# Kernel optimization log

Hardware: AMD Instinct MI355X
Metric: run time of the kernel (lower is better)

The kernel has to match this reference:

```python
import jax, jax.numpy as jnp
import numpy as np
from jax import lax

B, T = 64, 200
NUM_C, DIM_S, SIZE_M = 2000, 128, 50


def setup_inputs() -> dict:
    key = jax.random.key(0)
    ks = jax.random.split(key, 12)
    d = {}
    d['skill'] = jax.random.randint(ks[0], (B, T), 0, NUM_C)
    d['answer'] = jax.random.randint(ks[1], (B, T), 0, 2)
    s = 1.0 / np.sqrt(DIM_S)
    d['k_emb'] = jax.random.normal(ks[2], (NUM_C + 1, DIM_S), jnp.float32)
    d['v_emb'] = jax.random.normal(ks[3], (2 * NUM_C + 1, DIM_S), jnp.float32)
    # kaiming_normal on [size_m, dim_s]: std = sqrt(2/dim_s)
    d['Mk'] = jax.random.normal(ks[4], (SIZE_M, DIM_S), jnp.float32) * np.sqrt(2.0 / DIM_S)
    d['Mv0'] = jax.random.normal(ks[5], (SIZE_M, DIM_S), jnp.float32) * np.sqrt(2.0 / DIM_S)
    d['f_W'] = jax.random.normal(ks[6], (DIM_S, 2 * DIM_S), jnp.float32) * (1.0 / np.sqrt(2 * DIM_S))
    d['f_b'] = jnp.zeros((DIM_S,), jnp.float32)
    d['p_W'] = jax.random.normal(ks[7], (NUM_C, DIM_S), jnp.float32) * s
    d['p_b'] = jnp.zeros((NUM_C,), jnp.float32)
    d['e_W'] = jax.random.normal(ks[8], (DIM_S, DIM_S), jnp.float32) * s
    d['e_b'] = jnp.zeros((DIM_S,), jnp.float32)
    d['a_W'] = jax.random.normal(ks[9], (DIM_S, DIM_S), jnp.float32) * s
    d['a_b'] = jnp.zeros((DIM_S,), jnp.float32)
    return d


def reference(skill, answer, k_emb, v_emb, Mk, Mv0, f_W, f_b, p_W, p_b, e_W, e_b, a_W, a_b):
    num_c = p_W.shape[0]
    bsz = skill.shape[0]
    answer_x = jnp.where(answer == 2, 1, answer)
    x = skill + num_c * answer_x                       # [B,T]
    k = k_emb[skill]                                   # [B,T,D]
    v = v_emb[x]                                       # [B,T,D]
    w = jax.nn.softmax(jnp.einsum('btd,md->btm', k, Mk), axis=-1)   # [B,T,M]
    e = jax.nn.sigmoid(jnp.einsum('btd,ed->bte', v, e_W) + e_b)      # [B,T,D]
    a = jnp.tanh(jnp.einsum('btd,ed->bte', v, a_W) + a_b)            # [B,T,D]

    Mv_init = jnp.broadcast_to(Mv0, (bsz,) + Mv0.shape)              # [B,M,D]

    def step(Mvt, inp):
        et, at, wt = inp                               # [B,D],[B,D],[B,M]
        # read uses pre-update memory (Mv[:, :-1] in the torch code)
        read = jnp.einsum('bm,bmd->bd', wt, Mvt)
        Mvt_new = Mvt * (1.0 - wt[:, :, None] * et[:, None, :]) + wt[:, :, None] * at[:, None, :]
        return Mvt_new, read

    _, reads = lax.scan(step, Mv_init,
                        (e.transpose(1, 0, 2), a.transpose(1, 0, 2), w.transpose(1, 0, 2)))
    reads = reads.transpose(1, 0, 2)                   # [B,T,D]

    f = jnp.tanh(jnp.concatenate([reads, k], axis=-1) @ f_W.T + f_b)  # [B,T,D]
    p = jax.nn.sigmoid(f @ p_W.T + p_b)                # [B,T,num_c] (dropout is identity at eval)
    p = p[:, :-1, :]
    next_skill = skill[:, 1:]                          # [B,T-1]
    idx = jnp.minimum(next_skill, num_c - 1)
    pred = jnp.take_along_axis(p, idx[..., None], axis=-1)[..., 0]
    pred = jnp.where(next_skill < num_c, pred, 0.0)    # index num_c -> zero row in torch one_hot
    return pred
```

## Files before the change

### kernel.cpp

```cpp
#include <hip/hip_runtime.h>
#include <math.h>

#define Bsz 64
#define Tn 200
#define NUMC 2000
#define DS 128
#define SM 50
#define NTOK (Bsz*Tn)
#define WVS 10
#define MPG 10

typedef __attribute__((ext_vector_type(8))) short bfrag;
typedef __attribute__((ext_vector_type(4))) float f32x4;
typedef __attribute__((ext_vector_type(4))) unsigned int u32x4;

__device__ __forceinline__ unsigned short f2bf(float x) {
    unsigned int u = __builtin_bit_cast(unsigned int, x);
    u = u + 0x7fffu + ((u >> 16) & 1u);
    return (unsigned short)(u >> 16);
}
__device__ __forceinline__ unsigned int pack2(float a, float b) {
    return (unsigned int)f2bf(a) | ((unsigned int)f2bf(b) << 16);
}
__device__ __forceinline__ bfrag mk_frag(f32x4 x, f32x4 y) {
    u32x4 t;
    t[0] = pack2(x[0], x[1]); t[1] = pack2(x[2], x[3]);
    t[2] = pack2(y[0], y[1]); t[3] = pack2(y[2], y[3]);
    return __builtin_bit_cast(bfrag, t);
}

__device__ __forceinline__ float fast_exp(float x)  { return __builtin_amdgcn_exp2f(x * 1.44269504f); }
__device__ __forceinline__ float fast_rcp(float x)  { return __builtin_amdgcn_rcpf(x); }
__device__ __forceinline__ float fast_sigmoid(float x) { return fast_rcp(1.f + fast_exp(-x)); }
__device__ __forceinline__ float fast_tanh(float x) { return 1.f - 2.f * fast_rcp(fast_exp(2.f * x) + 1.f); }

__global__ __launch_bounds__(256) void k0_cast(
    const float* __restrict__ eW, const float* __restrict__ aW,
    const float* __restrict__ fW, const float* __restrict__ Mk,
    unsigned int* __restrict__ BeaU, unsigned int* __restrict__ BkmU,
    unsigned int* __restrict__ Bf0U)
{
    const int g = blockIdx.x * 256 + threadIdx.x;
    if (g >= 9216) return;
    int gm, mat;
    unsigned int* dst;
    if (g < 4096)      { mat = 0; gm = g;        dst = BeaU; }
    else if (g < 7168) { mat = 1; gm = g - 4096; dst = BkmU; }
    else               { mat = 2; gm = g - 7168; dst = Bf0U; }
    const int nt = gm >> 8, r = gm & 255, ki = r >> 6, L = r & 63;
    const int n = nt * 16 + (L & 15);
    const int k = ki * 32 + (L >> 4) * 8;

    const float* src = nullptr;
    if (mat == 0) {
        src = (n < 128) ? (eW + (size_t)n * DS + k) : (aW + (size_t)(n - 128) * DS + k);
    } else if (mat == 1) {
        if (n < 128)      src = fW + (size_t)n * (2 * DS) + DS + k;
        else if (n < 128 + SM) src = Mk + (size_t)(n - 128) * DS + k;
    } else {
        src = fW + (size_t)n * (2 * DS) + k;
    }
    float v[8];
    #pragma unroll
    for (int j = 0; j < 8; j++) v[j] = src ? src[j] : 0.f;
    u32x4 o;
    o[0] = pack2(v[0], v[1]); o[1] = pack2(v[2], v[3]);
    o[2] = pack2(v[4], v[5]); o[3] = pack2(v[6], v[7]);
    ((u32x4*)dst)[gm] = o;
}

__global__ __launch_bounds__(64, 4) void k1_gemm(
    const int* __restrict__ skill, const int* __restrict__ answer,
    const float* __restrict__ k_emb, const float* __restrict__ v_emb,
    const unsigned int* __restrict__ BeaU, const unsigned int* __restrict__ BkmU,
    const float* __restrict__ eB, const float* __restrict__ aB,
    float* __restrict__ w_buf, float* __restrict__ e_buf,
    float* __restrict__ a_buf, float* __restrict__ kp_buf)
{
    const int bid = blockIdx.x;
    const int tile = bid / 7, role = bid % 7;
    const int L = threadIdx.x, L15 = L & 15, quad = L >> 4;
    const int tok0 = tile * 16;
    const int tokA = tok0 + L15;
    const int row0 = tok0 + quad * 4;

    const int s = skill[tokA];
    const float* ap;
    if (role < 4) {
        const int an = answer[tokA];
        const int ax = (an == 2) ? 1 : an;
        ap = v_emb + ((size_t)(s + NUMC * ax)) * DS + quad * 8;
    } else {
        ap = k_emb + (size_t)s * DS + quad * 8;
    }
    bfrag Af[4];
    #pragma unroll
    for (int ki = 0; ki < 4; ki++) {
        const f32x4* a4 = (const f32x4*)(ap + ki * 32);
        Af[ki] = mk_frag(a4[0], a4[1]);
    }

    const bfrag* Bp = (role < 4) ? (const bfrag*)BeaU : (const bfrag*)BkmU;
    const int g0 = (role < 4) ? role * 4 : (role - 4) * 4;

    f32x4 acc[4];
    #pragma unroll
    for (int t = 0; t < 4; t++) acc[t] = (f32x4){0.f,0.f,0.f,0.f};

    #pragma unroll
    for (int half = 0; half < 2; half++) {
        bfrag bh[2][4];
        #pragma unroll
        for (int tt = 0; tt < 2; tt++)
            #pragma unroll
            for (int ki = 0; ki < 4; ki++)
                bh[tt][ki] = Bp[(size_t)((g0 + half * 2 + tt) * 4 + ki) * 64 + L];
        #pragma unroll
        for (int ki = 0; ki < 4; ki++)
            #pragma unroll
            for (int tt = 0; tt < 2; tt++)
                acc[half * 2 + tt] = __builtin_amdgcn_mfma_f32_16x16x32_bf16(
                    Af[ki], bh[tt][ki], acc[half * 2 + tt], 0, 0, 0);
    }

    if (role == 6) {
        #pragma unroll
        for (int reg = 0; reg < 4; reg++) {
            float mx = -1e30f;
            #pragma unroll
            for (int t = 0; t < 4; t++) { const int c = t * 16 + L15; if (c < SM) mx = fmaxf(mx, acc[t][reg]); }
            #pragma unroll
            for (int msk = 1; msk <= 8; msk <<= 1) mx = fmaxf(mx, __shfl_xor(mx, msk));
            float ex[4]; float ssum = 0.f;
            #pragma unroll
            for (int t = 0; t < 4; t++) {
                const int c = t * 16 + L15;
                ex[t] = (c < SM) ? fast_exp(acc[t][reg] - mx) : 0.f;
                ssum += ex[t];
            }
            #pragma unroll
            for (int msk = 1; msk <= 8; msk <<= 1) ssum += __shfl_xor(ssum, msk);
            const float inv = fast_rcp(ssum);
            float* wp = w_buf + (size_t)(row0 + reg) * SM;
            #pragma unroll
            for (int t = 0; t < 4; t++) { const int c = t * 16 + L15; if (c < SM) wp[c] = ex[t] * inv; }
        }
    } else {
        const int nb = (role & 1) * 64;
        float* obuf = (role < 2) ? e_buf : (role < 4) ? a_buf : kp_buf;
        const float* bias = (role < 2) ? eB : aB;
        #pragma unroll
        for (int t = 0; t < 4; t++) {
            const int n = nb + t * 16 + L15;
            const float bv = (role < 4) ? bias[n] : 0.f;
            #pragma unroll
            for (int reg = 0; reg < 4; reg++) {
                float v = acc[t][reg] + bv;
                if (role < 2)      v = fast_sigmoid(v);
                else if (role < 4) v = fast_tanh(v);
                obuf[(size_t)(row0 + reg) * DS + n] = v;
            }
        }
    }
}

__global__ __launch_bounds__(640) void k2_scan(
    const float* __restrict__ w_buf, const float* __restrict__ e_buf,
    const float* __restrict__ a_buf, const float* __restrict__ Mv0,
    unsigned short* __restrict__ reads)
{
    const int bi   = blockIdx.x;
    const int b    = bi >> 1;
    const int dh   = bi & 1;
    const int tid  = threadIdx.x;
    const int wv   = tid >> 6;
    const int L    = tid & 63;
    const int d    = dh * 64 + L;
    const int m0   = wv * MPG;
    const int base = b * Tn;

    const int mg   = wv;
    const int m0e  = mg * 5;

    __shared__ float red[2][WVS][8][64];

    float Mv[5];
    #pragma unroll
    for (int m = 0; m < 5; m++) Mv[m] = Mv0[(size_t)(m0e + m) * DS + d];

    float se[4][2], sa[4][2], sw[4][2][5];

    #define LOADST(ST, T)                                                      \
        { const int tc_ = ((T) < Tn) ? (T) : 0;                                \
          _Pragma("unroll")                                                    \
          for (int q_ = 0; q_ < 2; q_++) {                                     \
              const int tf_ = base + tc_ + q_;                                 \
              se[ST][q_] = e_buf[(size_t)tf_*DS + d];                          \
              sa[ST][q_] = a_buf[(size_t)tf_*DS + d];                          \
              _Pragma("unroll")                                                \
              for (int m_ = 0; m_ < 5; m_++)                                   \
                  sw[ST][q_][m_] = w_buf[(size_t)tf_*SM + m0e + m_];           \
          } }

    LOADST(0, 0) LOADST(1, 2) LOADST(2, 4) LOADST(3, 6)

    for (int i = 0; i < 25; i++) {
        const int tb = i * 8;
        const int p  = i & 1;
        #pragma unroll
        for (int sub = 0; sub < 4; sub++) {
            const int t0 = tb + sub * 2;
            #pragma unroll
            for (int q = 0; q < 2; q++) {
                const float ev = se[sub][q], av = sa[sub][q];
                float rd = 0.f;
                #pragma unroll
                for (int m = 0; m < 5; m++) {
                    const float wm = sw[sub][q][m];
                    rd = fmaf(wm, Mv[m], rd);
                    Mv[m] = fmaf(-wm, fmaf(ev, Mv[m], -av), Mv[m]);
                }
                red[p][wv][sub * 2 + q][L] = rd;
            }
            LOADST(sub, t0 + 8)
        }
        __syncthreads();
        if (tid < 512) {
            const int tt = tid >> 6, dd = tid & 63;
            float s = red[p][0][tt][dd];
            #pragma unroll
            for (int g = 1; g < WVS; g++) s += red[p][g][tt][dd];
            reads[(size_t)(base + tb + tt) * DS + dh * 64 + dd] = f2bf(s);
        }
    }
    #undef LOADST
}

__global__ __launch_bounds__(128, 2) void k3_gemm(
    const unsigned short* __restrict__ reads, const float* __restrict__ kp_buf,
    const unsigned int* __restrict__ Bf0U, const float* __restrict__ fB,
    const float* __restrict__ pW, const float* __restrict__ pB,
    const int* __restrict__ skill, float* __restrict__ out)
{
    const int tid = threadIdx.x;
    const int wv  = tid >> 6;
    const int L   = tid & 63, L15 = L & 15, quad = L >> 4;
    const int tok0 = blockIdx.x * 16;
    const int tokA = tok0 + L15;
    const int row0 = tok0 + quad * 4;

    __shared__ float sm[2][16];

    bfrag Rf[4];
    #pragma unroll
    for (int ki = 0; ki < 4; ki++)
        Rf[ki] = *(const bfrag*)(reads + (size_t)tokA * DS + ki * 32 + quad * 8);

    const bfrag* Bf0 = (const bfrag*)Bf0U;
    const int g0 = wv * 4;

    f32x4 acc[4];
    #pragma unroll
    for (int t = 0; t < 4; t++) acc[t] = (f32x4){0.f,0.f,0.f,0.f};

    #pragma unroll
    for (int half = 0; half < 2; half++) {
        bfrag bh[2][4];
        #pragma unroll
        for (int tt = 0; tt < 2; tt++)
            #pragma unroll
            for (int ki = 0; ki < 4; ki++)
                bh[tt][ki] = Bf0[(size_t)((g0 + half * 2 + tt) * 4 + ki) * 64 + L];
        #pragma unroll
        for (int ki = 0; ki < 4; ki++)
            #pragma unroll
            for (int tt = 0; tt < 2; tt++)
                acc[half * 2 + tt] = __builtin_amdgcn_mfma_f32_16x16x32_bf16(
                    Rf[ki], bh[tt][ki], acc[half * 2 + tt], 0, 0, 0);
    }

    const int nb = wv * 64;
    float f[4][4];
    #pragma unroll
    for (int t = 0; t < 4; t++) {
        const int n = nb + t * 16 + L15;
        const float fb = fB[n];
        #pragma unroll
        for (int reg = 0; reg < 4; reg++)
            f[reg][t] = fast_tanh(acc[t][reg] + kp_buf[(size_t)(row0 + reg) * DS + n] + fb);
    }

    #pragma unroll
    for (int reg = 0; reg < 4; reg++) {
        const int tok = row0 + reg;
        const int t = tok % Tn;
        const bool act = (t < Tn - 1);
        float contrib = 0.f;
        if (act) {
            const int sn = skill[tok + 1];
            const int ix = (sn < NUMC) ? sn : (NUMC - 1);
            const float* pr = pW + (size_t)ix * DS + nb + L15;
            #pragma unroll
            for (int t4 = 0; t4 < 4; t4++)
                contrib = fmaf(f[reg][t4], pr[t4 * 16], contrib);
        }
        #pragma unroll
        for (int msk = 1; msk <= 8; msk <<= 1)
            contrib += __shfl_xor(contrib, msk);
        if (L15 == 0) sm[wv][quad * 4 + reg] = contrib;
    }
    __syncthreads();
    if (tid < 16) {
        const int tok = tok0 + tid;
        const int t = tok % Tn;
        if (t < Tn - 1) {
            const int sn = skill[tok + 1];
            const int ix = (sn < NUMC) ? sn : (NUMC - 1);
            const float val = sm[0][tid] + sm[1][tid] + pB[ix];
            out[(size_t)(tok / Tn) * (Tn - 1) + t] = (sn < NUMC) ? fast_sigmoid(val) : 0.f;
        }
    }
}

extern "C" void kernel_launch(void* const* d_in, const int* in_sizes, int n_in,
                              void* d_out, int out_size, void* d_ws, size_t ws_size,
                              hipStream_t stream)
{
    const int*   skill  = (const int*)  d_in[0];
    const int*   answer = (const int*)  d_in[1];
    const float* k_emb  = (const float*)d_in[2];
    const float* v_emb  = (const float*)d_in[3];
    const float* Mk     = (const float*)d_in[4];
    const float* Mv0    = (const float*)d_in[5];
    const float* f_W    = (const float*)d_in[6];
    const float* f_b    = (const float*)d_in[7];
    const float* p_W    = (const float*)d_in[8];
    const float* p_b    = (const float*)d_in[9];
    const float* e_W    = (const float*)d_in[10];
    const float* e_b    = (const float*)d_in[11];
    const float* a_W    = (const float*)d_in[12];
    const float* a_b    = (const float*)d_in[13];
    float* out = (float*)d_out;

    float* ws     = (float*)d_ws;
    float* w_buf  = ws;
    float* e_buf  = w_buf  + (size_t)NTOK*SM;
    float* a_buf  = e_buf  + (size_t)NTOK*DS;
    float* kp_buf = a_buf  + (size_t)NTOK*DS;
    unsigned short* reads = (unsigned short*)(kp_buf + (size_t)NTOK*DS);
    unsigned int* BeaU = (unsigned int*)(reads + (size_t)NTOK*DS);
    unsigned int* BkmU = BeaU + 4096 * 4;
    unsigned int* Bf0U = BkmU + 3072 * 4;

    k0_cast<<<36, 256, 0, stream>>>(e_W, a_W, f_W, Mk, BeaU, BkmU, Bf0U);
    k1_gemm<<<7*(NTOK/16), 64, 0, stream>>>(skill, answer, k_emb, v_emb,
        BeaU, BkmU, e_b, a_b, w_buf, e_buf, a_buf, kp_buf);
    k2_scan<<<Bsz*2, 640, 0, stream>>>(w_buf, e_buf, a_buf, Mv0, reads);
    k3_gemm<<<NTOK/16, 128, 0, stream>>>(reads, kp_buf, Bf0U, f_b,
        p_W, p_b, skill, out);
}
```

Before: 147.4 us.

## Stage scan inputs in double-buffered LDS chunks with cooperative coalesced loads

The recurrent memory scan now loads e, a and w for 40-timestep chunks cooperatively across the block into double-buffered shared memory. Register prefetch then reads from LDS instead of issuing scattered global loads per timestep. The next chunk's global loads are issued into registers before the current chunk is computed and are written to LDS afterward. This aims to hide global latency on the serial critical path, at the cost of more LDS use, extra barriers and register pressure.

```diff
diff --git a/kernel.cpp b/kernel.cpp
--- a/kernel.cpp
+++ b/kernel.cpp
@@ -8,7 +8,8 @@
 #define SM 50
 #define NTOK (Bsz*Tn)
 #define WVS 10
-#define MPG 10
+#define CH 40
+#define NCH (Tn/CH)
 
 typedef __attribute__((ext_vector_type(8))) short bfrag;
 typedef __attribute__((ext_vector_type(4))) float f32x4;
@@ -176,61 +177,118 @@
     const int wv   = tid >> 6;
     const int L    = tid & 63;
     const int d    = dh * 64 + L;
-    const int m0   = wv * MPG;
+    const int m0e  = wv * 5;
     const int base = b * Tn;
 
-    const int mg   = wv;
-    const int m0e  = mg * 5;
-
+    __shared__ float se_s[2][CH][64];
+    __shared__ float sa_s[2][CH][64];
+    __shared__ float sw_s[2][CH * SM];
     __shared__ float red[2][WVS][8][64];
 
     float Mv[5];
     #pragma unroll
     for (int m = 0; m < 5; m++) Mv[m] = Mv0[(size_t)(m0e + m) * DS + d];
 
+    const int r0 = tid >> 6, c0 = tid & 63;
+
+    {
+        const size_t ebase = (size_t)base * DS + dh * 64 + c0;
+        #pragma unroll
+        for (int pp = 0; pp < 4; pp++) {
+            const int row = pp * 10 + r0;
+            se_s[0][row][c0] = e_buf[ebase + (size_t)row * DS];
+            sa_s[0][row][c0] = a_buf[ebase + (size_t)row * DS];
+        }
+        const int wbase = base * SM;
+        #pragma unroll
+        for (int pp = 0; pp < 4; pp++) {
+            const int j = tid + pp * 640;
+            if (j < CH * SM) sw_s[0][j] = w_buf[wbase + j];
+        }
+    }
+    __syncthreads();
+
     float se[4][2], sa[4][2], sw[4][2][5];
-
-    #define LOADST(ST, T)                                                      \
-        { const int tc_ = ((T) < Tn) ? (T) : 0;                                \
-          _Pragma("unroll")                                                    \
-          for (int q_ = 0; q_ < 2; q_++) {                                     \
-              const int tf_ = base + tc_ + q_;                                 \
-              se[ST][q_] = e_buf[(size_t)tf_*DS + d];                          \
-              sa[ST][q_] = a_buf[(size_t)tf_*DS + d];                          \
-              _Pragma("unroll")                                                \
-              for (int m_ = 0; m_ < 5; m_++)                                   \
-                  sw[ST][q_][m_] = w_buf[(size_t)tf_*SM + m0e + m_];           \
-          } }
-
-    LOADST(0, 0) LOADST(1, 2) LOADST(2, 4) LOADST(3, 6)
-
-    for (int i = 0; i < 25; i++) {
-        const int tb = i * 8;
-        const int p  = i & 1;
-        #pragma unroll
-        for (int sub = 0; sub < 4; sub++) {
-            const int t0 = tb + sub * 2;
-            #pragma unroll
-            for (int q = 0; q < 2; q++) {
-                const float ev = se[sub][q], av = sa[sub][q];
-                float rd = 0.f;
+    int p = 0;
+
+    #define LOADST(ST, TL)                                                     \
+        { const int tl_ = (TL);                                                \
+          if (tl_ < CH) {                                                      \
+            _Pragma("unroll")                                                  \
+            for (int q_ = 0; q_ < 2; q_++) {                                   \
+                se[ST][q_] = se_s[p][tl_ + q_][L];                             \
+                sa[ST][q_] = sa_s[p][tl_ + q_][L];                             \
+                _Pragma("unroll")                                              \
+                for (int m_ = 0; m_ < 5; m_++)                                 \
+                    sw[ST][q_][m_] = sw_s[p][(tl_ + q_) * SM + m0e + m_];      \
+            } } }
+
+    for (int c = 0; c < NCH; c++) {
+        float st_e[4], st_a[4], st_w[4];
+        if (c + 1 < NCH) {
+            const int tcn = (c + 1) * CH;
+            const size_t ebase = (size_t)(base + tcn) * DS + dh * 64 + c0;
+            #pragma unroll
+            for (int pp = 0; pp < 4; pp++) {
+                const int row = pp * 10 + r0;
+                st_e[pp] = e_buf[ebase + (size_t)row * DS];
+                st_a[pp] = a_buf[ebase + (size_t)row * DS];
+            }
+            const int wbase = (base + tcn) * SM;
+            #pragma unroll
+            for (int pp = 0; pp < 4; pp++) {
+                const int j = tid + pp * 640;
+                if (j < CH * SM) st_w[pp] = w_buf[wbase + j];
+            }
+        }
+
+        LOADST(0, 0) LOADST(1, 2) LOADST(2, 4) LOADST(3, 6)
+
+        #pragma unroll 1
+        for (int ti = 0; ti < 5; ti++) {
+            const int tlb = ti * 8;
+            const int gi  = c * 5 + ti;
+            const int pr  = gi & 1;
+            #pragma unroll
+            for (int sub = 0; sub < 4; sub++) {
                 #pragma unroll
-                for (int m = 0; m < 5; m++) {
-                    const float wm = sw[sub][q][m];
-                    rd = fmaf(wm, Mv[m], rd);
-                    Mv[m] = fmaf(-wm, fmaf(ev, Mv[m], -av), Mv[m]);
+                for (int q = 0; q < 2; q++) {
+                    const float ev = se[sub][q], av = sa[sub][q];
+                    float rd = 0.f;
+                    #pragma unroll
+                    for (int m = 0; m < 5; m++) {
+                        const float wm = sw[sub][q][m];
+                        rd = fmaf(wm, Mv[m], rd);
+                        Mv[m] = fmaf(-wm, fmaf(ev, Mv[m], -av), Mv[m]);
+                    }
+                    red[pr][wv][sub * 2 + q][L] = rd;
                 }
-                red[p][wv][sub * 2 + q][L] = rd;
-            }
-            LOADST(sub, t0 + 8)
-        }
-        __syncthreads();
-        if (tid < 512) {
-            const int tt = tid >> 6, dd = tid & 63;
-            float s = red[p][0][tt][dd];
-            #pragma unroll
-            for (int g = 1; g < WVS; g++) s += red[p][g][tt][dd];
-            reads[(size_t)(base + tb + tt) * DS + dh * 64 + dd] = f2bf(s);
+                LOADST(sub, tlb + sub * 2 + 8)
+            }
+            __syncthreads();
+            if (tid < 512) {
+                const int tt = tid >> 6, dd = tid & 63;
+                float s = red[pr][0][tt][dd];
+                #pragma unroll
+                for (int g = 1; g < WVS; g++) s += red[pr][g][tt][dd];
+                reads[(size_t)(base + c * CH + tlb + tt) * DS + dh * 64 + dd] = f2bf(s);
+            }
+        }
+
+        if (c + 1 < NCH) {
+            #pragma unroll
+            for (int pp = 0; pp < 4; pp++) {
+                const int row = pp * 10 + r0;
+                se_s[p ^ 1][row][c0] = st_e[pp];
+                sa_s[p ^ 1][row][c0] = st_a[pp];
+            }
+            #pragma unroll
+            for (int pp = 0; pp < 4; pp++) {
+                const int j = tid + pp * 640;
+                if (j < CH * SM) sw_s[p ^ 1][j] = st_w[pp];
+            }
+            __syncthreads();
+            p ^= 1;
         }
     }
     #undef LOADST
```

Measured after the change: 138.9 us. 1.06x faster.

## Restructure memory scan to 4 waves with padded weight layout and LDS staging

Applied to the files above, without the earlier changes.

The scan kernel drops from 10 waves of 5 memory slots to 4 waves of 13 slots each, so there are fewer partial sums to reduce. The attention weights are now written in a padded 64-wide layout that groups each wave's slots, and they are staged through double-buffered shared memory and read with vector loads. The cross-wave reduction is vectorised over 4 timesteps and writes 8 timesteps per sync. The trade-off is longer serial dependency chains per thread and lower occupancy per block, in exchange for less reduction traffic and fewer global loads.

```diff
diff --git a/kernel.cpp b/kernel.cpp
--- a/kernel.cpp
+++ b/kernel.cpp
@@ -7,8 +7,6 @@
 #define DS 128
 #define SM 50
 #define NTOK (Bsz*Tn)
-#define WVS 10
-#define MPG 10
 
 typedef __attribute__((ext_vector_type(8))) short bfrag;
 typedef __attribute__((ext_vector_type(4))) float f32x4;
@@ -74,7 +72,7 @@
     const float* __restrict__ k_emb, const float* __restrict__ v_emb,
     const unsigned int* __restrict__ BeaU, const unsigned int* __restrict__ BkmU,
     const float* __restrict__ eB, const float* __restrict__ aB,
-    float* __restrict__ w_buf, float* __restrict__ e_buf,
+    float* __restrict__ w2, float* __restrict__ e_buf,
     float* __restrict__ a_buf, float* __restrict__ kp_buf)
 {
     const int bid = blockIdx.x;
@@ -141,9 +139,20 @@
             #pragma unroll
             for (int msk = 1; msk <= 8; msk <<= 1) ssum += __shfl_xor(ssum, msk);
             const float inv = fast_rcp(ssum);
-            float* wp = w_buf + (size_t)(row0 + reg) * SM;
-            #pragma unroll
-            for (int t = 0; t < 4; t++) { const int c = t * 16 + L15; if (c < SM) wp[c] = ex[t] * inv; }
+            float* wp = w2 + (size_t)(row0 + reg) * 64;
+            #pragma unroll
+            for (int t = 0; t < 4; t++) {
+                const int c = t * 16 + L15;
+                const int idx = (c < 13) ? c
+                              : (c < 26) ? c + 3
+                              : (c < 38) ? c + 6
+                              : (c < 50) ? c + 10
+                              : (c < 53) ? c - 37
+                              : (c < 56) ? c - 24
+                              : (c < 60) ? c - 12
+                              : c;
+                wp[idx] = ex[t] * inv;
+            }
         }
     } else {
         const int nb = (role & 1) * 64;
@@ -164,8 +173,8 @@
     }
 }
 
-__global__ __launch_bounds__(640) void k2_scan(
-    const float* __restrict__ w_buf, const float* __restrict__ e_buf,
+__global__ __launch_bounds__(256) void k2_scan(
+    const float* __restrict__ w2, const float* __restrict__ e_buf,
     const float* __restrict__ a_buf, const float* __restrict__ Mv0,
     unsigned short* __restrict__ reads)
 {
@@ -176,64 +185,97 @@
     const int wv   = tid >> 6;
     const int L    = tid & 63;
     const int d    = dh * 64 + L;
-    const int m0   = wv * MPG;
     const int base = b * Tn;
-
-    const int mg   = wv;
-    const int m0e  = mg * 5;
-
-    __shared__ float red[2][WVS][8][64];
-
-    float Mv[5];
-    #pragma unroll
-    for (int m = 0; m < 5; m++) Mv[m] = Mv0[(size_t)(m0e + m) * DS + d];
-
-    float se[4][2], sa[4][2], sw[4][2][5];
-
-    #define LOADST(ST, T)                                                      \
-        { const int tc_ = ((T) < Tn) ? (T) : 0;                                \
-          _Pragma("unroll")                                                    \
-          for (int q_ = 0; q_ < 2; q_++) {                                     \
-              const int tf_ = base + tc_ + q_;                                 \
-              se[ST][q_] = e_buf[(size_t)tf_*DS + d];                          \
-              sa[ST][q_] = a_buf[(size_t)tf_*DS + d];                          \
-              _Pragma("unroll")                                                \
-              for (int m_ = 0; m_ < 5; m_++)                                   \
-                  sw[ST][q_][m_] = w_buf[(size_t)tf_*SM + m0e + m_];           \
-          } }
-
-    LOADST(0, 0) LOADST(1, 2) LOADST(2, 4) LOADST(3, 6)
-
-    for (int i = 0; i < 25; i++) {
-        const int tb = i * 8;
-        const int p  = i & 1;
-        #pragma unroll
-        for (int sub = 0; sub < 4; sub++) {
-            const int t0 = tb + sub * 2;
-            #pragma unroll
-            for (int q = 0; q < 2; q++) {
-                const float ev = se[sub][q], av = sa[sub][q];
-                float rd = 0.f;
+    const int gbase  = wv * 16;
+    const int mstart = (wv == 0) ? 0 : (wv == 1) ? 13 : (wv == 2) ? 26 : 38;
+
+    __shared__ __align__(16) float red[2][4][64][12];
+    __shared__ __align__(16) float wt_s[2][8][64];
+
+    float Mv[13];
+    #pragma unroll
+    for (int j = 0; j < 13; j++) {
+        const int m = mstart + j;
+        Mv[j] = (m < SM) ? Mv0[(size_t)m * DS + d] : 0.f;
+    }
+
+    float re[2][4], ra[2][4];
+    #define LOADEA(SL, T)                                                  \
+        { const int t_ = (T);                                              \
+          if (t_ < Tn) {                                                   \
+            _Pragma("unroll")                                              \
+            for (int i_ = 0; i_ < 4; i_++) {                               \
+                re[SL][i_] = e_buf[(size_t)(base + t_ + i_) * DS + d];     \
+                ra[SL][i_] = a_buf[(size_t)(base + t_ + i_) * DS + d];     \
+            } } }
+
+    const int r0 = tid >> 6, c0 = tid & 63;
+
+    #pragma unroll
+    for (int ps = 0; ps < 2; ps++)
+        wt_s[0][ps * 4 + r0][c0] = w2[(size_t)(base + ps * 4 + r0) * 64 + c0];
+    LOADEA(0, 0) LOADEA(1, 4)
+    __syncthreads();
+
+    int cur = 0;
+    for (int ti = 0; ti < 25; ti++) {
+        const int tb = ti * 8;
+        const int pr = ti & 1;
+
+        float wst[2];
+        if (ti < 24) {
+            #pragma unroll
+            for (int ps = 0; ps < 2; ps++)
+                wst[ps] = w2[(size_t)(base + tb + 8 + ps * 4 + r0) * 64 + c0];
+        }
+
+        #pragma unroll
+        for (int g = 0; g < 2; g++) {
+            f32x4 rd;
+            #pragma unroll
+            for (int it = 0; it < 4; it++) {
+                const int tl = g * 4 + it;
+                const float* wp = &wt_s[cur][tl][gbase];
+                const f32x4 wa = *(const f32x4*)wp;
+                const f32x4 wb = *(const f32x4*)(wp + 4);
+                const f32x4 wc = *(const f32x4*)(wp + 8);
+                const float wd = wp[12];
+                const float ev = re[g][it], av = ra[g][it];
+                float r = 0.f;
                 #pragma unroll
-                for (int m = 0; m < 5; m++) {
-                    const float wm = sw[sub][q][m];
-                    rd = fmaf(wm, Mv[m], rd);
-                    Mv[m] = fmaf(-wm, fmaf(ev, Mv[m], -av), Mv[m]);
+                for (int j = 0; j < 13; j++) {
+                    const float wm = (j < 4) ? wa[j] : (j < 8) ? wb[j - 4]
+                                   : (j < 12) ? wc[j - 8] : wd;
+                    r = fmaf(wm, Mv[j], r);
+                    Mv[j] = fmaf(-wm, fmaf(ev, Mv[j], -av), Mv[j]);
                 }
-                red[p][wv][sub * 2 + q][L] = rd;
+                rd[it] = r;
             }
-            LOADST(sub, t0 + 8)
+            *(f32x4*)&red[pr][wv][L][g * 4] = rd;
+            LOADEA(g, tb + g * 4 + 8)
+        }
+
+        if (ti < 24) {
+            #pragma unroll
+            for (int ps = 0; ps < 2; ps++)
+                wt_s[cur ^ 1][ps * 4 + r0][c0] = wst[ps];
         }
         __syncthreads();
-        if (tid < 512) {
-            const int tt = tid >> 6, dd = tid & 63;
-            float s = red[p][0][tt][dd];
-            #pragma unroll
-            for (int g = 1; g < WVS; g++) s += red[p][g][tt][dd];
-            reads[(size_t)(base + tb + tt) * DS + dh * 64 + dd] = f2bf(s);
-        }
-    }
-    #undef LOADST
+
+        if (tid < 128) {
+            const int th = tid >> 6;
+            const int dd = tid & 63;
+            f32x4 s = *(const f32x4*)&red[pr][0][dd][th * 4];
+            #pragma unroll
+            for (int g2 = 1; g2 < 4; g2++)
+                s += *(const f32x4*)&red[pr][g2][dd][th * 4];
+            #pragma unroll
+            for (int i = 0; i < 4; i++)
+                reads[(size_t)(base + tb + th * 4 + i) * DS + dh * 64 + dd] = f2bf(s[i]);
+        }
+        cur ^= 1;
+    }
+    #undef LOADEA
 }
 
 __global__ __launch_bounds__(128, 2) void k3_gemm(
@@ -343,8 +385,8 @@
     float* out = (float*)d_out;
 
     float* ws     = (float*)d_ws;
-    float* w_buf  = ws;
-    float* e_buf  = w_buf  + (size_t)NTOK*SM;
+    float* w2     = ws;
+    float* e_buf  = w2     + (size_t)NTOK*64;
     float* a_buf  = e_buf  + (size_t)NTOK*DS;
     float* kp_buf = a_buf  + (size_t)NTOK*DS;
     unsigned short* reads = (unsigned short*)(kp_buf + (size_t)NTOK*DS);
@@ -354,8 +396,8 @@
 
     k0_cast<<<36, 256, 0, stream>>>(e_W, a_W, f_W, Mk, BeaU, BkmU, Bf0U);
     k1_gemm<<<7*(NTOK/16), 64, 0, stream>>>(skill, answer, k_emb, v_emb,
-        BeaU, BkmU, e_b, a_b, w_buf, e_buf, a_buf, kp_buf);
-    k2_scan<<<Bsz*2, 640, 0, stream>>>(w_buf, e_buf, a_buf, Mv0, reads);
+        BeaU, BkmU, e_b, a_b, w2, e_buf, a_buf, kp_buf);
+    k2_scan<<<Bsz*2, 256, 0, stream>>>(w2, e_buf, a_buf, Mv0, reads);
     k3_gemm<<<NTOK/16, 128, 0, stream>>>(reads, kp_buf, Bf0U, f_b,
         p_W, p_b, skill, out);
 }
```

Result: faster. 138.8 us (-5.8%).

## Restructure scan to single-wave blocks with shuffle reduction and padded weight layout

Applied to the files above, without the earlier changes.

The memory scan kernel moves from 128 blocks of 10 waves, which reduced partial reads through shared memory with a barrier every 8 steps, to 512 single-wave blocks. Each lane owns 13 memory slots for one of 16 d columns, and the 4 slot groups are combined with cross-lane shuffles. The softmax weights are stored in a padded 64-wide layout so each slot group's 13 weights load as vector reads. This removes block-wide barriers and shared-memory reductions and spreads the work over more CUs, at the cost of more registers per lane, three padding slots that do redundant work, and an extra shuffle reduction every step.

```diff
diff --git a/kernel.cpp b/kernel.cpp
--- a/kernel.cpp
+++ b/kernel.cpp
@@ -7,8 +7,6 @@
 #define DS 128
 #define SM 50
 #define NTOK (Bsz*Tn)
-#define WVS 10
-#define MPG 10
 
 typedef __attribute__((ext_vector_type(8))) short bfrag;
 typedef __attribute__((ext_vector_type(4))) float f32x4;
@@ -74,7 +72,7 @@
     const float* __restrict__ k_emb, const float* __restrict__ v_emb,
     const unsigned int* __restrict__ BeaU, const unsigned int* __restrict__ BkmU,
     const float* __restrict__ eB, const float* __restrict__ aB,
-    float* __restrict__ w_buf, float* __restrict__ e_buf,
+    float* __restrict__ w2, float* __restrict__ e_buf,
     float* __restrict__ a_buf, float* __restrict__ kp_buf)
 {
     const int bid = blockIdx.x;
@@ -141,9 +139,20 @@
             #pragma unroll
             for (int msk = 1; msk <= 8; msk <<= 1) ssum += __shfl_xor(ssum, msk);
             const float inv = fast_rcp(ssum);
-            float* wp = w_buf + (size_t)(row0 + reg) * SM;
-            #pragma unroll
-            for (int t = 0; t < 4; t++) { const int c = t * 16 + L15; if (c < SM) wp[c] = ex[t] * inv; }
+            float* wp = w2 + (size_t)(row0 + reg) * 64;
+            #pragma unroll
+            for (int t = 0; t < 4; t++) {
+                const int c = t * 16 + L15;
+                const int idx = (c < 13) ? c
+                              : (c < 26) ? c + 3
+                              : (c < 39) ? c + 6
+                              : (c < 50) ? c + 9
+                              : (c < 53) ? c - 37
+                              : (c < 56) ? c - 24
+                              : (c < 59) ? c - 11
+                              : c;
+                wp[idx] = ex[t] * inv;
+            }
         }
     } else {
         const int nb = (role & 1) * 64;
@@ -164,76 +173,78 @@
     }
 }
 
-__global__ __launch_bounds__(640) void k2_scan(
-    const float* __restrict__ w_buf, const float* __restrict__ e_buf,
+__global__ __launch_bounds__(64) void k2_scan(
+    const float* __restrict__ w2, const float* __restrict__ e_buf,
     const float* __restrict__ a_buf, const float* __restrict__ Mv0,
     unsigned short* __restrict__ reads)
 {
-    const int bi   = blockIdx.x;
-    const int b    = bi >> 1;
-    const int dh   = bi & 1;
-    const int tid  = threadIdx.x;
-    const int wv   = tid >> 6;
-    const int L    = tid & 63;
-    const int d    = dh * 64 + L;
-    const int m0   = wv * MPG;
+    const int bid  = blockIdx.x;
+    const int b    = bid >> 3;
+    const int dseg = bid & 7;
+    const int lane = threadIdx.x;
+    const int mg   = lane >> 4;
+    const int dd   = lane & 15;
+    const int d    = dseg * 16 + dd;
+    const int mstart = mg * 13;
+    const int gcol = mg * 16;
     const int base = b * Tn;
 
-    const int mg   = wv;
-    const int m0e  = mg * 5;
-
-    __shared__ float red[2][WVS][8][64];
-
-    float Mv[5];
-    #pragma unroll
-    for (int m = 0; m < 5; m++) Mv[m] = Mv0[(size_t)(m0e + m) * DS + d];
-
-    float se[4][2], sa[4][2], sw[4][2][5];
-
-    #define LOADST(ST, T)                                                      \
-        { const int tc_ = ((T) < Tn) ? (T) : 0;                                \
+    float Mv[13];
+    #pragma unroll
+    for (int j = 0; j < 13; j++) {
+        const int m = (mstart + j < SM) ? (mstart + j) : (SM - 1);
+        Mv[j] = Mv0[(size_t)m * DS + d];
+    }
+
+    float ev[2][4], av[2][4], wd[2][4];
+    f32x4 wa[2][4], wb[2][4], wc[2][4];
+
+    #define LOADS(S, T0)                                                       \
+        { _Pragma("unroll")                                                    \
+          for (int i_ = 0; i_ < 4; i_++) {                                     \
+              const int t_ = (T0) + i_;                                        \
+              const int tc_ = (t_ < Tn) ? t_ : 0;                              \
+              ev[S][i_] = e_buf[(size_t)(base + tc_) * DS + d];                \
+              av[S][i_] = a_buf[(size_t)(base + tc_) * DS + d];                \
+              const float* wp_ = w2 + (size_t)(base + tc_) * 64 + gcol;        \
+              wa[S][i_] = *(const f32x4*)wp_;                                  \
+              wb[S][i_] = *(const f32x4*)(wp_ + 4);                            \
+              wc[S][i_] = *(const f32x4*)(wp_ + 8);                            \
+              wd[S][i_] = wp_[12];                                             \
+          } }
+
+    #define PROC4(S, T0)                                                       \
+        { float r4[4];                                                         \
           _Pragma("unroll")                                                    \
-          for (int q_ = 0; q_ < 2; q_++) {                                     \
-              const int tf_ = base + tc_ + q_;                                 \
-              se[ST][q_] = e_buf[(size_t)tf_*DS + d];                          \
-              sa[ST][q_] = a_buf[(size_t)tf_*DS + d];                          \
+          for (int it = 0; it < 4; it++) {                                     \
+              const float ev_ = ev[S][it], av_ = av[S][it];                    \
+              float rd = 0.f;                                                  \
               _Pragma("unroll")                                                \
-              for (int m_ = 0; m_ < 5; m_++)                                   \
-                  sw[ST][q_][m_] = w_buf[(size_t)tf_*SM + m0e + m_];           \
-          } }
-
-    LOADST(0, 0) LOADST(1, 2) LOADST(2, 4) LOADST(3, 6)
-
-    for (int i = 0; i < 25; i++) {
-        const int tb = i * 8;
-        const int p  = i & 1;
-        #pragma unroll
-        for (int sub = 0; sub < 4; sub++) {
-            const int t0 = tb + sub * 2;
-            #pragma unroll
-            for (int q = 0; q < 2; q++) {
-                const float ev = se[sub][q], av = sa[sub][q];
-                float rd = 0.f;
-                #pragma unroll
-                for (int m = 0; m < 5; m++) {
-                    const float wm = sw[sub][q][m];
-                    rd = fmaf(wm, Mv[m], rd);
-                    Mv[m] = fmaf(-wm, fmaf(ev, Mv[m], -av), Mv[m]);
-                }
-                red[p][wv][sub * 2 + q][L] = rd;
-            }
-            LOADST(sub, t0 + 8)
-        }
-        __syncthreads();
-        if (tid < 512) {
-            const int tt = tid >> 6, dd = tid & 63;
-            float s = red[p][0][tt][dd];
-            #pragma unroll
-            for (int g = 1; g < WVS; g++) s += red[p][g][tt][dd];
-            reads[(size_t)(base + tb + tt) * DS + dh * 64 + dd] = f2bf(s);
-        }
-    }
-    #undef LOADST
+              for (int j = 0; j < 13; j++) {                                   \
+                  const float wm = (j < 4) ? wa[S][it][j]                      \
+                                 : (j < 8) ? wb[S][it][j - 4]                  \
+                                 : (j < 12) ? wc[S][it][j - 8]                 \
+                                 : wd[S][it];                                  \
+                  rd = fmaf(wm, Mv[j], rd);                        \
+                  Mv[j] = fmaf(-wm, fmaf(ev_, Mv[j], -av_), Mv[j]);            \
+              }                                                                \
+              rd += __shfl_xor(rd, 16);                                        \
+              rd += __shfl_xor(rd, 32);                                        \
+              r4[it] = rd;                                                     \
+          }                                                                    \
+          const float val = (mg == 0) ? r4[0] : (mg == 1) ? r4[1]              \
+                          : (mg == 2) ? r4[2] : r4[3];                         \
+          reads[(size_t)(base + (T0) + mg) * DS + d] = f2bf(val); }
+
+    LOADS(0, 0) LOADS(1, 4)
+
+    for (int blk = 0; blk < 25; blk++) {
+        const int t0 = blk * 8;
+        PROC4(0, t0)     LOADS(0, t0 + 8)
+        PROC4(1, t0 + 4) LOADS(1, t0 + 12)
+    }
+    #undef LOADS
+    #undef PROC4
 }
 
 __global__ __launch_bounds__(128, 2) void k3_gemm(
@@ -343,8 +354,8 @@
     float* out = (float*)d_out;
 
     float* ws     = (float*)d_ws;
-    float* w_buf  = ws;
-    float* e_buf  = w_buf  + (size_t)NTOK*SM;
+    float* w2     = ws;
+    float* e_buf  = w2     + (size_t)NTOK*64;
     float* a_buf  = e_buf  + (size_t)NTOK*DS;
     float* kp_buf = a_buf  + (size_t)NTOK*DS;
     unsigned short* reads = (unsigned short*)(kp_buf + (size_t)NTOK*DS);
@@ -354,8 +365,8 @@
 
     k0_cast<<<36, 256, 0, stream>>>(e_W, a_W, f_W, Mk, BeaU, BkmU, Bf0U);
     k1_gemm<<<7*(NTOK/16), 64, 0, stream>>>(skill, answer, k_emb, v_emb,
-        BeaU, BkmU, e_b, a_b, w_buf, e_buf, a_buf, kp_buf);
-    k2_scan<<<Bsz*2, 640, 0, stream>>>(w_buf, e_buf, a_buf, Mv0, reads);
+        BeaU, BkmU, e_b, a_b, w2, e_buf, a_buf, kp_buf);
+    k2_scan<<<Bsz*8, 64, 0, stream>>>(w2, e_buf, a_buf, Mv0, reads);
     k3_gemm<<<NTOK/16, 128, 0, stream>>>(reads, kp_buf, Bf0U, f_b,
         p_W, p_b, skill, out);
 }
```

Result: faster. 137.5 us (-6.7%).
